# Performance work log

Measured on AMD Instinct MI355X. Metric: run time of the kernel, lower is better.

## Reference

```python
import jax, jax.numpy as jnp
import numpy as np

B, N1, R12, R23 = 1, 4096, 4, 4
N2, N3 = N1 * R12, N1 * R12 * R23
D, F, H, NCLS, K = 1024, 512, 256, 4, 256


def setup_inputs() -> dict:
    key = jax.random.key(0)
    ks = jax.random.split(key, 10)
    s = 0.02
    return {
        "x1": jax.random.normal(ks[0], (B, N1, D), jnp.float32),
        "x2": jax.random.normal(ks[1], (B, N2, D), jnp.float32),
        "x3": jax.random.normal(ks[2], (B, N3, D), jnp.float32),
        # 3 fc layers (low/mid/high mag): Linear(D->F)
        "fcW": (jax.random.normal(ks[3], (3, D, F), jnp.float32) * s),
        "fcb": jnp.zeros((3, F), jnp.float32),
        # 5 gated-attention modules: 0=ga_low,1=ga_mid,2=ga_high,3=aux_low,4=aux_mid
        "gaWa": (jax.random.normal(ks[4], (5, F, H), jnp.float32) * s),
        "gaba": jnp.zeros((5, H), jnp.float32),
        "gaWb": (jax.random.normal(ks[5], (5, F, H), jnp.float32) * s),
        "gabb": jnp.zeros((5, H), jnp.float32),
        "gaWc": (jax.random.normal(ks[6], (5, H, 1), jnp.float32) * s),
        "gabc": jnp.zeros((5, 1), jnp.float32),
        "Wh": (jax.random.normal(ks[7], (F, NCLS), jnp.float32) * s),
        "bh": jnp.zeros((NCLS,), jnp.float32),
        "k_sample": K,
    }


def _ga(x, i, Wa, ba, Wb, bb, Wc, bc):
    # GatedAttention: tanh branch * sigmoid branch -> Linear(H->1); returns (B,N)
    a = jnp.tanh(x @ Wa[i] + ba[i])
    g = jax.nn.sigmoid(x @ Wb[i] + bb[i])
    return ((a * g) @ Wc[i] + bc[i])[..., 0]


def _block_gather(x, idx, ratio):
    # Equivalent to einsum('bkn,bnd->bkd', kron(one_hot(idx), eye(ratio)), x):
    # pick contiguous blocks of `ratio` rows for each selected coarse index.
    b, n, d = x.shape
    xb = x.reshape(b, n // ratio, ratio, d)
    out = jnp.take_along_axis(xb, idx[:, :, None, None], axis=1)  # (B,k,ratio,D)
    return out.reshape(b, idx.shape[1] * ratio, d)


def reference(x1, x2, x3, fcW, fcb, gaWa, gaba, gaWb, gabb, gaWc, gabc, Wh, bh, k_sample):
    ga = (gaWa, gaba, gaWb, gabb, gaWc, gabc)
    n1, n2, n3 = x1.shape[1], x2.shape[1], x3.shape[1]

    # --- low mag ---
    h1 = jax.nn.relu(x1 @ fcW[0] + fcb[0])                    # (B,N1,F)
    A1 = jax.nn.softmax(_ga(h1, 0, *ga), axis=-1)             # (B,N1)
    M1 = jnp.einsum('bn,bnf->bf', A1, h1)                     # (B,F)
    A1_aux = jax.nn.softmax(_ga(h1, 3, *ga), axis=-1)
    k1 = min(n1, int(k_sample))
    idx1 = jnp.sort(jax.lax.top_k(A1_aux, k1)[1], axis=-1)    # (B,k1)

    # zoom: gather selected blocks from mid and high mag features
    x2s = _block_gather(x2, idx1, n2 // n1)                   # (B,k1*R12,D)
    x3s = _block_gather(x3, idx1, n3 // n1)                   # (B,k1*R12*R23,D)

    # --- mid mag ---
    h2 = jax.nn.relu(x2s @ fcW[1] + fcb[1])
    A2 = jax.nn.softmax(_ga(h2, 1, *ga), axis=-1)
    M2 = jnp.einsum('bn,bnf->bf', A2, h2)
    A2_aux = jax.nn.softmax(_ga(h2, 4, *ga), axis=-1)
    k2 = min(h2.shape[1], int(k_sample))
    idx2 = jnp.sort(jax.lax.top_k(A2_aux, k2)[1], axis=-1)

    x3s2 = _block_gather(x3s, idx2, n3 // n2)                 # (B,k2*R23,D)

    # --- high mag ---
    h3 = jax.nn.relu(x3s2 @ fcW[2] + fcb[2])
    A3 = jax.nn.softmax(_ga(h3, 2, *ga), axis=-1)
    M3 = jnp.einsum('bn,bnf->bf', A3, h3)

    M = M1 + M2 + M3                                           # (B,F)
    logits = M @ Wh + bh                                       # (B,NCLS)
    return logits
```

## Files before the change

kernel.cpp:

```cpp
#include <hip/hip_runtime.h>
#include <hip/hip_bf16.h>
#include <math.h>


typedef __attribute__((ext_vector_type(8))) short short8;
typedef __attribute__((ext_vector_type(4))) float float4a;

__device__ __forceinline__ ushort f2bf(float f) {
    unsigned u = __float_as_uint(f);
    return (ushort)((u + 0x7fffu + ((u >> 16) & 1u)) >> 16);
}
__device__ __forceinline__ uint pk2(float a, float b) {
    __hip_bfloat162 t = __float22bfloat162_rn(make_float2(a, b));
    uint u; __builtin_memcpy(&u, &t, 4); return u;
}
__device__ __forceinline__ float aload(const float* p) {
    return __hip_atomic_load(p, __ATOMIC_RELAXED, __HIP_MEMORY_SCOPE_AGENT);
}

template<int SPLIT>
__global__ __launch_bounds__(256) void zm_hgemm(
    const float* __restrict__ A, int lda,
    const int* __restrict__ rowmap,
    const ushort* __restrict__ Bt,
    const float* __restrict__ bias,
    float* __restrict__ Cf, ushort* __restrict__ Cb, int ldc, int K)
{
    __shared__ ushort As[128 * 40];
    __shared__ ushort Bs[64 * 40];
    const int tid = threadIdx.x;
    const int brow = blockIdx.y << 7;
    const int bcol = blockIdx.x << 6;
    const int kbeg = SPLIT ? ((int)blockIdx.z << 8) : 0;
    const int kend = SPLIT ? kbeg + 256 : K;

    const int sr = tid >> 1;
    const int sk = (tid & 1) << 4;
    int arow = brow + sr;
    if (rowmap) arow = rowmap[arow];
    const float* Ap = A + (size_t)arow * lda;

    const int bn = tid >> 2;
    const int bk = (tid & 3) << 3;
    const ushort* Bp = Bt + (size_t)(bcol + bn) * K + bk;

    const int w = tid >> 6;
    const int wm = (w >> 1) << 6;
    const int wn = (w & 1) << 5;
    const int lane = tid & 63;
    const int lm = lane & 15;
    const int lq = lane >> 4;

    float4a acc[4][2] = {};

    for (int k0 = kbeg; k0 < kend; k0 += 32) {
        const float* ap = Ap + k0 + sk;
        float4 v0 = *(const float4*)(ap);
        float4 v1 = *(const float4*)(ap + 4);
        float4 v2 = *(const float4*)(ap + 8);
        float4 v3 = *(const float4*)(ap + 12);
        uint4 p0, p1;
        p0.x = pk2(v0.x, v0.y); p0.y = pk2(v0.z, v0.w);
        p0.z = pk2(v1.x, v1.y); p0.w = pk2(v1.z, v1.w);
        p1.x = pk2(v2.x, v2.y); p1.y = pk2(v2.z, v2.w);
        p1.z = pk2(v3.x, v3.y); p1.w = pk2(v3.z, v3.w);
        *(uint4*)&As[sr * 40 + sk]     = p0;
        *(uint4*)&As[sr * 40 + sk + 8] = p1;
        *(uint4*)&Bs[bn * 40 + bk] = *(const uint4*)(Bp + k0);
        __syncthreads();
        short8 afr[4], bfr[2];
#pragma unroll
        for (int mt = 0; mt < 4; mt++)
            afr[mt] = *(const short8*)&As[(wm + mt * 16 + lm) * 40 + lq * 8];
#pragma unroll
        for (int nt = 0; nt < 2; nt++)
            bfr[nt] = *(const short8*)&Bs[(wn + nt * 16 + lm) * 40 + lq * 8];
#pragma unroll
        for (int mt = 0; mt < 4; mt++)
#pragma unroll
            for (int nt = 0; nt < 2; nt++)
                acc[mt][nt] = __builtin_amdgcn_mfma_f32_16x16x32_bf16(
                    afr[mt], bfr[nt], acc[mt][nt], 0, 0, 0);
        __syncthreads();
    }

#pragma unroll
    for (int mt = 0; mt < 4; mt++) {
#pragma unroll
        for (int nt = 0; nt < 2; nt++) {
            int gc = bcol + wn + nt * 16 + lm;
            float bv = bias[gc];
            if (SPLIT && blockIdx.z != 0) bv = 0.0f;
#pragma unroll
            for (int r = 0; r < 4; r++) {
                int gr = brow + wm + mt * 16 + lq * 4 + r;
                float v = acc[mt][nt][r] + bv;
                if (SPLIT) {
                    atomicAdd(&Cf[(size_t)gr * ldc + gc], v);
                } else {
                    v = fmaxf(v, 0.0f);
                    Cf[(size_t)gr * ldc + gc] = v;
                    Cb[(size_t)gr * ldc + gc] = f2bf(v);
                }
            }
        }
    }
}

template<int AMODE>
__global__ __launch_bounds__(256) void zm_sgemm(
    const void* __restrict__ Av, int lda,
    const ushort* __restrict__ Bt,
    const float* __restrict__ bint,
    const float* __restrict__ wc0, const float* __restrict__ wc1,
    float* __restrict__ sMain, float* __restrict__ sAux,
    float* __restrict__ statsOut, int* __restrict__ cnt2, int lastBlk)
{
    __shared__ ushort As[64 * 40];
    __shared__ ushort Bs[64 * 40];
    __shared__ float part[4][64];
    const int tid = threadIdx.x;
    const int brow = blockIdx.y << 6;
    const int bcol = blockIdx.x << 6;

    const int sr = tid >> 2;
    const int sk = (tid & 3) << 3;
    const float*  Af = (const float*)Av;
    const ushort* Ab = (const ushort*)Av;
    const ushort* Bp = Bt + (size_t)(bcol + sr) * 512 + sk;

    const int w = tid >> 6;
    const int wn = w << 4;
    const int lane = tid & 63;
    const int lm = lane & 15;
    const int lq = lane >> 4;

    float4a acc[4] = {};

    for (int k0 = 0; k0 < 512; k0 += 32) {
        if (AMODE == 0) {
            *(uint4*)&As[sr * 40 + sk] =
                *(const uint4*)(Ab + (size_t)(brow + sr) * lda + k0 + sk);
        } else {
            const float* ap = Af + (size_t)(brow + sr) * lda + k0 + sk;
            float4 v0 = *(const float4*)ap;
            float4 v1 = *(const float4*)(ap + 4);
            v0.x = fmaxf(v0.x, 0.f); v0.y = fmaxf(v0.y, 0.f);
            v0.z = fmaxf(v0.z, 0.f); v0.w = fmaxf(v0.w, 0.f);
            v1.x = fmaxf(v1.x, 0.f); v1.y = fmaxf(v1.y, 0.f);
            v1.z = fmaxf(v1.z, 0.f); v1.w = fmaxf(v1.w, 0.f);
            uint4 pk;
            pk.x = pk2(v0.x, v0.y); pk.y = pk2(v0.z, v0.w);
            pk.z = pk2(v1.x, v1.y); pk.w = pk2(v1.z, v1.w);
            *(uint4*)&As[sr * 40 + sk] = pk;
        }
        *(uint4*)&Bs[sr * 40 + sk] = *(const uint4*)(Bp + k0);
        __syncthreads();
        short8 bfr = *(const short8*)&Bs[(wn + lm) * 40 + lq * 8];
#pragma unroll
        for (int mt = 0; mt < 4; mt++) {
            short8 afr = *(const short8*)&As[(mt * 16 + lm) * 40 + lq * 8];
            acc[mt] = __builtin_amdgcn_mfma_f32_16x16x32_bf16(afr, bfr, acc[mt], 0, 0, 0);
        }
        __syncthreads();
    }

    const int gc = bcol + wn + lm;
    const float* wcp = (gc >= 512) ? wc1 : wc0;
    const float wcv = wcp[(gc & 511) >> 1];
    const float bv = bint[gc];
    const bool odd = (gc & 1);
    float* sp = (bcol >= 512) ? sAux : sMain;

#pragma unroll
    for (int mt = 0; mt < 4; mt++) {
        float red[4];
#pragma unroll
        for (int r = 0; r < 4; r++) {
            float v = acc[mt][r] + bv;
            float x = odd ? (1.0f / (1.0f + expf(-v))) : tanhf(v);
            float prt = __shfl_xor(x, 1);
            float ctr = odd ? 0.0f : (x * prt * wcv);
            ctr += __shfl_xor(ctr, 1);
            ctr += __shfl_xor(ctr, 2);
            ctr += __shfl_xor(ctr, 4);
            ctr += __shfl_xor(ctr, 8);
            red[r] = ctr;
        }
        if (lm == 0) {
#pragma unroll
            for (int r = 0; r < 4; r++) part[w][mt * 16 + lq * 4 + r] = red[r];
        }
    }
    __syncthreads();
    if (tid < 64) {
        float tot = part[0][tid] + part[1][tid] + part[2][tid] + part[3][tid];
        atomicAdd(&sp[brow + tid], tot);
    }

    if (statsOut) {
        __threadfence();
        __shared__ int lastf;
        if (tid == 0)
            lastf = (__hip_atomic_fetch_add(cnt2, 1, __ATOMIC_ACQ_REL,
                                            __HIP_MEMORY_SCOPE_AGENT) == lastBlk);
        __syncthreads();
        if (lastf) {
            float* red = (float*)part;
            float vv[4];
            float mx = -3.4e38f;
#pragma unroll
            for (int j = 0; j < 4; j++) {
                vv[j] = aload(&sMain[tid + j * 256]);
                mx = fmaxf(mx, vv[j]);
            }
            red[tid] = mx; __syncthreads();
            for (int o = 128; o > 0; o >>= 1) {
                if (tid < o) red[tid] = fmaxf(red[tid], red[tid + o]);
                __syncthreads();
            }
            mx = red[0]; __syncthreads();
            float z = 0.0f;
#pragma unroll
            for (int j = 0; j < 4; j++) z += expf(vv[j] - mx);
            red[tid] = z; __syncthreads();
            for (int o = 128; o > 0; o >>= 1) {
                if (tid < o) red[tid] += red[tid + o];
                __syncthreads();
            }
            if (tid == 0) { statsOut[0] = mx; statsOut[1] = red[0]; }
        }
    }
}

__global__ __launch_bounds__(1024) void zm_topk(
    const float* __restrict__ sa, const float* __restrict__ sm, int n,
    const int* __restrict__ idx_prev,
    int* __restrict__ idx_out, int* __restrict__ rm_out,
    float* __restrict__ stOut)
{
    __shared__ unsigned long long keys[4096];
    const int bs = 1024;
    const int tid = threadIdx.x;

    if (blockIdx.x == 1) {
        float* red = (float*)keys;
        float mx = -3.4e38f;
        for (int i = tid; i < n; i += bs) mx = fmaxf(mx, sm[i]);
        red[tid] = mx; __syncthreads();
        for (int o = 512; o > 0; o >>= 1) {
            if (tid < o) red[tid] = fmaxf(red[tid], red[tid + o]);
            __syncthreads();
        }
        mx = red[0]; __syncthreads();
        float z = 0.0f;
        for (int i = tid; i < n; i += bs) z += expf(sm[i] - mx);
        red[tid] = z; __syncthreads();
        for (int o = 512; o > 0; o >>= 1) {
            if (tid < o) red[tid] += red[tid + o];
            __syncthreads();
        }
        if (tid == 0) { stOut[0] = mx; stOut[1] = red[0]; }
        return;
    }

    for (int i = tid; i < n; i += bs) {
        unsigned u = __float_as_uint(sa[i]);
        u = (u & 0x80000000u) ? ~u : (u | 0x80000000u);
        keys[i] = ((unsigned long long)(~u) << 32) | (unsigned)i;
    }
    __syncthreads();
    for (int k2 = 2; k2 <= n; k2 <<= 1) {
        for (int j = k2 >> 1; j > 0; j >>= 1) {
            for (int i = tid; i < n; i += bs) {
                int ixj = i ^ j;
                if (ixj > i) {
                    unsigned long long a = keys[i], b = keys[ixj];
                    bool up = ((i & k2) == 0);
                    if ((a > b) == up) { keys[i] = b; keys[ixj] = a; }
                }
            }
            __syncthreads();
        }
    }
    int v = 0;
    if (tid < 256) v = (int)(keys[tid] & 0xffffffffu);
    __syncthreads();
    int* ik = (int*)keys;
    if (tid < 256) ik[tid] = v;
    __syncthreads();
    for (int k2 = 2; k2 <= 256; k2 <<= 1) {
        for (int j = k2 >> 1; j > 0; j >>= 1) {
            for (int i = tid; i < 256; i += bs) {
                int ixj = i ^ j;
                if (ixj > i) {
                    int a = ik[i], b = ik[ixj];
                    bool up = ((i & k2) == 0);
                    if ((a > b) == up) { ik[i] = b; ik[ixj] = a; }
                }
            }
            __syncthreads();
        }
    }
    if (tid < 256) idx_out[tid] = ik[tid];
    int t = ik[tid >> 2] * 4 + (tid & 3);
    rm_out[tid] = idx_prev ? (idx_prev[t >> 4] * 16 + (t & 15)) : t;
}

__global__ __launch_bounds__(256) void zm_prep(
    const float* __restrict__ fcW,
    const float* __restrict__ gaWa, const float* __restrict__ gaWb,
    const float* __restrict__ gaba, const float* __restrict__ gabb,
    ushort* __restrict__ fc_t, ushort* __restrict__ gint,
    float* __restrict__ bint, float4* __restrict__ zbase, int zn4)
{
    const int b = blockIdx.x;
    const int tid = threadIdx.x;
    if (b >= 2817) {
        float4 z4 = make_float4(0.f, 0.f, 0.f, 0.f);
        for (int i = (b - 2817) * 256 + tid; i < zn4; i += 64 * 256)
            zbase[i] = z4;
        return;
    }
    if (b == 2816) {
        for (int i = tid; i < 2560; i += 256) {
            int n, head;
            if (i < 1024)      { n = i;        head = (n >> 9) ? 3 : 0; }
            else if (i < 2048) { n = i - 1024; head = (n >> 9) ? 4 : 1; }
            else               { n = i - 2048; head = 2; }
            int h = (n & 511) >> 1;
            const float* src = (n & 1) ? gabb : gaba;
            bint[i] = src[head * 256 + h];
        }
        return;
    }
    __shared__ ushort tile[32][33];
    const int c = tid & 31, r8 = tid >> 5;
    if (b < 1536) {
        int mat = b >> 9, rem = b & 511;
        int tk = rem >> 4, tn = rem & 15;
        const float* src = fcW + (size_t)mat * 1024 * 512;
        ushort* dst = fc_t + (size_t)mat * 512 * 1024;
        int k0 = tk * 32, n0 = tn * 32;
#pragma unroll
        for (int it = 0; it < 4; it++) {
            int r = r8 + it * 8;
            tile[r][c] = f2bf(src[(size_t)(k0 + r) * 512 + n0 + c]);
        }
        __syncthreads();
#pragma unroll
        for (int it = 0; it < 4; it++) {
            int r = r8 + it * 8;
            dst[(size_t)(n0 + r) * 1024 + k0 + c] = tile[c][r];
        }
    } else {
        int idx = b - 1536;
        int mat = idx >> 7, rem = idx & 127;
        int tk = rem >> 3, th = rem & 7;
        int head = mat >> 1, br = mat & 1;
        const float* src = (br ? gaWb : gaWa) + (size_t)head * 512 * 256;
        ushort* dstb; int off;
        if (head == 0)      { dstb = gint;              off = 0;   }
        else if (head == 1) { dstb = gint + 1024 * 512; off = 0;   }
        else if (head == 2) { dstb = gint + 2048 * 512; off = 0;   }
        else if (head == 3) { dstb = gint;              off = 512; }
        else                { dstb = gint + 1024 * 512; off = 512; }
        int k0 = tk * 32, h0 = th * 32;
#pragma unroll
        for (int it = 0; it < 4; it++) {
            int r = r8 + it * 8;
            tile[r][c] = f2bf(src[(size_t)(k0 + r) * 256 + h0 + c]);
        }
        __syncthreads();
#pragma unroll
        for (int it = 0; it < 4; it++) {
            int r = r8 + it * 8;
            dstb[(size_t)(off + 2 * (h0 + r) + br) * 512 + k0 + c] = tile[c][r];
        }
    }
}

__global__ __launch_bounds__(256) void zm_final(
    const float* __restrict__ h1f, const float* __restrict__ h2f,
    const float* __restrict__ h3f,
    const float* __restrict__ s1, const float* __restrict__ s2,
    const float* __restrict__ s3,
    const float* __restrict__ st, float* __restrict__ Mbuf,
    int* __restrict__ cnt,
    const float* __restrict__ Wh, const float* __restrict__ bh,
    float* __restrict__ out)
{
    const int tid = threadIdx.x;
    const int b = blockIdx.x;
    const float* h; const float* s; const float* stp; int r0, rl;
    if (b < 64)      { h = h1f; s = s1; stp = st;     r0 = b * 64;        rl = 0; }
    else if (b < 80) { h = h2f; s = s2; stp = st + 2; r0 = (b - 64) * 64; rl = 1; }
    else             { h = h3f; s = s3; stp = st + 4; r0 = (b - 80) * 64; rl = 1; }
    const float mx = stp[0];
    const float invZ = 1.0f / stp[1];
    float a0 = 0.0f, a1 = 0.0f;
    for (int r = 0; r < 64; r++) {
        int n = r0 + r;
        float wgt = expf(s[n] - mx) * invZ;
        float v0 = h[(size_t)n * 512 + tid];
        float v1 = h[(size_t)n * 512 + 256 + tid];
        if (rl) { v0 = fmaxf(v0, 0.f); v1 = fmaxf(v1, 0.f); }
        a0 += wgt * v0; a1 += wgt * v1;
    }
    atomicAdd(&Mbuf[tid], a0);
    atomicAdd(&Mbuf[tid + 256], a1);
    __threadfence();
    __shared__ int lastf;
    if (tid == 0)
        lastf = (__hip_atomic_fetch_add(cnt, 1, __ATOMIC_ACQ_REL,
                                        __HIP_MEMORY_SCOPE_AGENT) == 95);
    __syncthreads();
    if (lastf) {
        const int c = tid >> 6, lane = tid & 63;
        float pacc = 0.0f;
        for (int f = lane; f < 512; f += 64)
            pacc += aload(&Mbuf[f]) * Wh[f * 4 + c];
        for (int o = 32; o > 0; o >>= 1) pacc += __shfl_down(pacc, o);
        if (lane == 0) out[c] = pacc + bh[c];
    }
}

extern "C" void kernel_launch(void* const* d_in, const int* in_sizes, int n_in,
                              void* d_out, int out_size, void* d_ws, size_t ws_size,
                              hipStream_t stream)
{
    const float* x1   = (const float*)d_in[0];
    const float* x2   = (const float*)d_in[1];
    const float* x3   = (const float*)d_in[2];
    const float* fcW  = (const float*)d_in[3];
    const float* fcb  = (const float*)d_in[4];
    const float* gaWa = (const float*)d_in[5];
    const float* gaba = (const float*)d_in[6];
    const float* gaWb = (const float*)d_in[7];
    const float* gabb = (const float*)d_in[8];
    const float* gaWc = (const float*)d_in[9];
    const float* Wh   = (const float*)d_in[11];
    const float* bh   = (const float*)d_in[12];
    float* out = (float*)d_out;

    char* p = (char*)d_ws;
    float*  h1f  = (float*)p;
    ushort* h1b  = (ushort*)(p + 8388608);
    ushort* fc_t = (ushort*)(p + 12582912);
    ushort* gint = (ushort*)(p + 15728640);
    float*  bint = (float*)(p + 18350080);
    float*  st   = (float*)(p + 18360320);
    int*    idx1 = (int*)(p + 18360352);
    int*    idx2 = (int*)(p + 18361376);
    int*    rm2  = (int*)(p + 18362400);
    int*    rm3  = (int*)(p + 18366496);
    char*   zbase = p + 18370592;
    float*  h2f  = (float*)zbase;
    float*  h3f  = (float*)(zbase + 2097152);
    float*  s1   = (float*)(zbase + 4194304);
    float*  s1a  = (float*)(zbase + 4210688);
    float*  s2   = (float*)(zbase + 4227072);
    float*  s2a  = (float*)(zbase + 4231168);
    float*  s3   = (float*)(zbase + 4235264);
    float*  Mbuf = (float*)(zbase + 4239360);
    int*    cnt  = (int*)(zbase + 4241408);
    const int ZN4 = 4241424 / 16;

    zm_prep<<<2881, 256, 0, stream>>>(fcW, gaWa, gaWb, gaba, gabb,
                                      fc_t, gint, bint, (float4*)zbase, ZN4);
    zm_hgemm<0><<<dim3(8, 32), 256, 0, stream>>>(x1, 1024, nullptr, fc_t, fcb,
                                                 h1f, h1b, 512, 1024);
    zm_sgemm<0><<<dim3(16, 64), 256, 0, stream>>>(h1b, 512, gint, bint,
                                                  gaWc, gaWc + 3 * 256,
                                                  s1, s1a, nullptr, nullptr, 0);
    zm_topk<<<2, 1024, 0, stream>>>(s1a, s1, 4096, nullptr, idx1, rm2, st);
    zm_hgemm<1><<<dim3(8, 8, 4), 256, 0, stream>>>(x2, 1024, rm2,
                                                   fc_t + 512 * 1024, fcb + 512,
                                                   h2f, nullptr, 512, 1024);
    zm_sgemm<1><<<dim3(16, 16), 256, 0, stream>>>(h2f, 512, gint + 1024 * 512,
                                                  bint + 1024,
                                                  gaWc + 256, gaWc + 4 * 256,
                                                  s2, s2a, nullptr, nullptr, 0);
    zm_topk<<<2, 1024, 0, stream>>>(s2a, s2, 1024, idx1, idx2, rm3, st + 2);
    zm_hgemm<1><<<dim3(8, 8, 4), 256, 0, stream>>>(x3, 1024, rm3,
                                                   fc_t + 2 * 512 * 1024, fcb + 1024,
                                                   h3f, nullptr, 512, 1024);
    zm_sgemm<1><<<dim3(8, 16), 256, 0, stream>>>(h3f, 512, gint + 2048 * 512,
                                                 bint + 2048,
                                                 gaWc + 2 * 256, gaWc + 2 * 256,
                                                 s3, s3, st + 4, cnt + 1, 127);
    zm_final<<<96, 256, 0, stream>>>(h1f, h2f, h3f, s1, s2, s3, st, Mbuf, cnt,
                                     Wh, bh, out);
}
```

Before: 604.3 us.

## Replace bitonic-sort top-k with radix-select threshold and prefix-scan compaction

The top-k kernel no longer bitonic-sorts all n keys and then re-sorts the 256 selected indices. Instead it runs a 4-pass 8-bit radix select with a shared histogram to find the k-th largest key. Selected indices are then written in ascending index order through a block-wide prefix scan of greater-than and equal counts, which removes many barrier-heavy sort stages. Ties at the threshold are resolved by taking the lowest indices. The per-thread key array is fixed at 4 entries, so n is assumed to be at most 4096.

```diff
diff --git a/kernel.cpp b/kernel.cpp
--- a/kernel.cpp
+++ b/kernel.cpp
@@ -239,71 +239,126 @@
     int* __restrict__ idx_out, int* __restrict__ rm_out,
     float* __restrict__ stOut)
 {
-    __shared__ unsigned long long keys[4096];
+    __shared__ float redf[1024];
+    __shared__ int hist[256];
+    __shared__ int idxbuf[256];
+    __shared__ int wsum[16];
+    __shared__ int bcastB, bcastAbove;
     const int bs = 1024;
     const int tid = threadIdx.x;
 
     if (blockIdx.x == 1) {
-        float* red = (float*)keys;
         float mx = -3.4e38f;
         for (int i = tid; i < n; i += bs) mx = fmaxf(mx, sm[i]);
-        red[tid] = mx; __syncthreads();
+        redf[tid] = mx; __syncthreads();
         for (int o = 512; o > 0; o >>= 1) {
-            if (tid < o) red[tid] = fmaxf(red[tid], red[tid + o]);
+            if (tid < o) redf[tid] = fmaxf(redf[tid], redf[tid + o]);
             __syncthreads();
         }
-        mx = red[0]; __syncthreads();
+        mx = redf[0]; __syncthreads();
         float z = 0.0f;
         for (int i = tid; i < n; i += bs) z += expf(sm[i] - mx);
-        red[tid] = z; __syncthreads();
+        redf[tid] = z; __syncthreads();
         for (int o = 512; o > 0; o >>= 1) {
-            if (tid < o) red[tid] += red[tid + o];
+            if (tid < o) redf[tid] += redf[tid + o];
             __syncthreads();
         }
-        if (tid == 0) { stOut[0] = mx; stOut[1] = red[0]; }
+        if (tid == 0) { stOut[0] = mx; stOut[1] = redf[0]; }
         return;
     }
 
-    for (int i = tid; i < n; i += bs) {
-        unsigned u = __float_as_uint(sa[i]);
-        u = (u & 0x80000000u) ? ~u : (u | 0x80000000u);
-        keys[i] = ((unsigned long long)(~u) << 32) | (unsigned)i;
-    }
+    const int ept = n >> 10;
+    const int lane = tid & 63;
+    unsigned key[4];
+#pragma unroll
+    for (int e = 0; e < 4; e++) key[e] = 0;
+    for (int e = 0; e < ept; e++) {
+        unsigned u = __float_as_uint(sa[tid * ept + e]);
+        key[e] = (u & 0x80000000u) ? ~u : (u | 0x80000000u);
+    }
+
+    unsigned prefix = 0;
+    int remaining = 256;
+    for (int pass = 0; pass < 4; pass++) {
+        const int shift = 24 - pass * 8;
+        if (tid < 256) hist[tid] = 0;
+        __syncthreads();
+        for (int e = 0; e < ept; e++) {
+            unsigned k = key[e];
+            bool ok = (pass == 0) || ((k >> (shift + 8)) == (prefix >> (shift + 8)));
+            if (ok) atomicAdd(&hist[(k >> shift) & 0xff], 1);
+        }
+        __syncthreads();
+        if (tid < 64) {
+            int h0 = hist[lane * 4 + 0], h1 = hist[lane * 4 + 1];
+            int h2 = hist[lane * 4 + 2], h3 = hist[lane * 4 + 3];
+            int q = h0 + h1 + h2 + h3;
+            int suf = q;
+#pragma unroll
+            for (int o = 1; o < 64; o <<= 1) {
+                int v = __shfl_down(suf, o);
+                if (lane + o < 64) suf += v;
+            }
+            int above = suf - q;
+            int c3 = above + h3;
+            int c2 = c3 + h2;
+            int c1 = c2 + h1;
+            int c0 = c1 + h0;
+            int cc[4]  = {c0, c1, c2, c3};
+            int nxt[4] = {c1, c2, c3, above};
+#pragma unroll
+            for (int j = 0; j < 4; j++)
+                if (cc[j] >= remaining && nxt[j] < remaining) {
+                    bcastB = lane * 4 + j;
+                    bcastAbove = nxt[j];
+                }
+        }
+        __syncthreads();
+        prefix |= ((unsigned)bcastB) << shift;
+        remaining -= bcastAbove;
+        __syncthreads();
+    }
+    const unsigned T = prefix;
+    const int m = remaining;
+
+    int gt = 0, eq = 0;
+    for (int e = 0; e < ept; e++) { gt += (key[e] > T); eq += (key[e] == T); }
+    int packed = (gt << 16) | eq;
+    int incl = packed;
+#pragma unroll
+    for (int o = 1; o < 64; o <<= 1) {
+        int v = __shfl_up(incl, o);
+        if (lane >= o) incl += v;
+    }
+    if (lane == 63) wsum[tid >> 6] = incl;
     __syncthreads();
-    for (int k2 = 2; k2 <= n; k2 <<= 1) {
-        for (int j = k2 >> 1; j > 0; j >>= 1) {
-            for (int i = tid; i < n; i += bs) {
-                int ixj = i ^ j;
-                if (ixj > i) {
-                    unsigned long long a = keys[i], b = keys[ixj];
-                    bool up = ((i & k2) == 0);
-                    if ((a > b) == up) { keys[i] = b; keys[ixj] = a; }
-                }
-            }
-            __syncthreads();
-        }
-    }
-    int v = 0;
-    if (tid < 256) v = (int)(keys[tid] & 0xffffffffu);
+    if (tid < 64) {
+        int v = (tid < 16) ? wsum[tid] : 0;
+        int s = v;
+#pragma unroll
+        for (int o = 1; o < 16; o <<= 1) {
+            int t2 = __shfl_up(s, o);
+            if (tid >= o) s += t2;
+        }
+        if (tid < 16) wsum[tid] = s - v;
+    }
     __syncthreads();
-    int* ik = (int*)keys;
-    if (tid < 256) ik[tid] = v;
+    int base = wsum[tid >> 6] + incl - packed;
+    int gt_before = base >> 16;
+    int eq_before = base & 0xffff;
+    for (int e = 0; e < ept; e++) {
+        if (key[e] > T) {
+            int eqa = (eq_before < m) ? eq_before : m;
+            idxbuf[gt_before + eqa] = tid * ept + e;
+            gt_before++;
+        } else if (key[e] == T) {
+            if (eq_before < m) idxbuf[gt_before + eq_before] = tid * ept + e;
+            eq_before++;
+        }
+    }
     __syncthreads();
-    for (int k2 = 2; k2 <= 256; k2 <<= 1) {
-        for (int j = k2 >> 1; j > 0; j >>= 1) {
-            for (int i = tid; i < 256; i += bs) {
-                int ixj = i ^ j;
-                if (ixj > i) {
-                    int a = ik[i], b = ik[ixj];
-                    bool up = ((i & k2) == 0);
-                    if ((a > b) == up) { ik[i] = b; ik[ixj] = a; }
-                }
-            }
-            __syncthreads();
-        }
-    }
-    if (tid < 256) idx_out[tid] = ik[tid];
-    int t = ik[tid >> 2] * 4 + (tid & 3);
+    if (tid < 256) idx_out[tid] = idxbuf[tid];
+    int t = idxbuf[tid >> 2] * 4 + (tid & 3);
     rm_out[tid] = idx_prev ? (idx_prev[t >> 4] * 16 + (t & 15)) : t;
 }
 
```

Measured after the change: 540.4 us. 1.12x faster.
